# Kernel optimization log

Hardware: AMD Instinct MI355X
Metric: run time of the kernel (lower is better)

Reference implementation:

```python
import jax, jax.numpy as jnp
import numpy as np

N_USERS = 50000
N_ITEMS = 50000
E = 400000
S = 128   # in_feats_s (memory / GRU hidden)
T = 64    # in_feats_t (time encoding dim)
ED = 64   # edge feature dim
M = 2 * S + T + ED  # in_feats_m = 384

_BASIS_FREQ = jnp.asarray(1.0 / 10 ** np.linspace(0, 9, T), dtype=jnp.float32)


def time_encode(ts):
    # cos(ts * freq + phase), phase == 0
    return jnp.cos(ts[:, None] * _BASIS_FREQ[None, :])


def mean_message(src_mem, dst_mem, ts, e, src, dst, n_dst):
    # mail per edge: [E, 2S + T + ED]
    mail = jnp.concatenate(
        [src_mem[src], dst_mem[dst], time_encode(ts), e], axis=1)
    s = jax.ops.segment_sum(mail, dst, num_segments=n_dst)
    cnt = jax.ops.segment_sum(jnp.ones_like(ts), dst, num_segments=n_dst)
    return s / jnp.maximum(cnt, 1.0)[:, None]


def gru_step(x, h, w_ih, w_hh, b_ih, b_hh):
    # single-step PyTorch GRU; gate order r, z, n
    gi = x @ w_ih.T + b_ih
    gh = h @ w_hh.T + b_hh
    ir, iz, i_n = jnp.split(gi, 3, axis=1)
    hr, hz, h_n = jnp.split(gh, 3, axis=1)
    r = jax.nn.sigmoid(ir + hr)
    z = jax.nn.sigmoid(iz + hz)
    n = jnp.tanh(i_n + r * h_n)
    return (1.0 - z) * n + z * h


def setup_inputs() -> dict:
    key = jax.random.key(0)
    ks = jax.random.split(key, 16)
    sc = 1.0 / np.sqrt(S)
    return {
        "si":   jax.random.normal(ks[0], (N_USERS, S), jnp.float32),
        "sj":   jax.random.normal(ks[1], (N_ITEMS, S), jnp.float32),
        "si_r": jax.random.normal(ks[2], (N_ITEMS, S), jnp.float32),
        "sj_r": jax.random.normal(ks[3], (N_USERS, S), jnp.float32),
        "t":    jax.random.uniform(ks[4], (E,), jnp.float32),
        "t_r":  jax.random.uniform(ks[5], (E,), jnp.float32),
        "e":    jax.random.normal(ks[6], (E, ED), jnp.float32),
        "e_r":  jax.random.normal(ks[7], (E, ED), jnp.float32),
        "w_ih": jax.random.normal(ks[8], (3 * S, M), jnp.float32) * sc,
        "w_hh": jax.random.normal(ks[9], (3 * S, S), jnp.float32) * sc,
        "b_ih": jax.random.normal(ks[10], (3 * S,), jnp.float32) * sc,
        "b_hh": jax.random.normal(ks[11], (3 * S,), jnp.float32) * sc,
        "src_g":  jax.random.randint(ks[12], (E,), 0, N_USERS, jnp.int32),
        "dst_g":  jax.random.randint(ks[13], (E,), 0, N_ITEMS, jnp.int32),
        "src_gr": jax.random.randint(ks[14], (E,), 0, N_ITEMS, jnp.int32),
        "dst_gr": jax.random.randint(ks[15], (E,), 0, N_USERS, jnp.int32),
    }


def reference(si, sj, si_r, sj_r, t, t_r, e, e_r,
              w_ih, w_hh, b_ih, b_hh,
              src_g, dst_g, src_gr, dst_gr):
    # g: user -> item; g_r: item -> user
    mj = mean_message(si, sj, t, e, src_g, dst_g, N_ITEMS)       # messages to items
    mi = mean_message(si_r, sj_r, t_r, e_r, src_gr, dst_gr, N_USERS)  # messages to users
    si_out = gru_step(mi, sj_r, w_ih, w_hh, b_ih, b_hh)  # user memory update
    sj_out = gru_step(mj, sj, w_ih, w_hh, b_ih, b_hh)    # item memory update
    return (si_out, sj_out)
```

## Files before the change

kernel.cpp:

```cpp
#include <hip/hip_runtime.h>
#include <math.h>

#define NUSERS 50000
#define NITEMS 50000
#define NTOT   100000
#define NNODE  50000
#define NCHUNK 196
#define MTILES 6250
#define KDIM   512
#define NWAVES 8192

typedef __attribute__((ext_vector_type(4))) float f32x4;
typedef __attribute__((ext_vector_type(8))) short short8;
typedef unsigned int u32;

#define AS1 __attribute__((address_space(1)))
#define AS3 __attribute__((address_space(3)))

static __device__ __forceinline__ unsigned short f2bf(float f) {
  unsigned int u = __float_as_uint(f);
  u += 0x7fffu + ((u >> 16) & 1u);
  return (unsigned short)(u >> 16);
}

static __device__ __forceinline__ u32 pack2(float x, float y) {
  return (u32)f2bf(x) | ((u32)f2bf(y) << 16);
}

static __device__ __forceinline__ void gload_lds16(const void* g, void* l) {
  __builtin_amdgcn_global_load_lds((const AS1 u32*)g, (AS3 u32*)l, 16, 0, 0);
}

__global__ void pack_w_kernel(const float* __restrict__ w_ih,
                              const float* __restrict__ w_hh,
                              const float* __restrict__ b_ih,
                              const float* __restrict__ b_hh,
                              unsigned short* __restrict__ Wb,
                              float* __restrict__ bb) {
  int idx = blockIdx.x * 256 + threadIdx.x;
  int j = idx & 7, l = (idx >> 3) & 63, ktt = idx >> 9;
  int kt = ktt & 15, tt = ktt >> 4;
  int g = tt * 16 + (l & 15);
  int k = kt * 32 + (l >> 4) * 8 + j;
  float v;
  if (g < 256)      v = (k < 384) ? w_ih[g * 384 + k] : w_hh[g * 128 + (k - 384)];
  else if (g < 384) v = (k < 384) ? w_ih[g * 384 + k] : 0.0f;
  else              v = (k < 384) ? 0.0f : w_hh[(g - 128) * 128 + (k - 384)];
  Wb[idx] = f2bf(v);
  if (idx < 512) {
    float b = (idx < 256) ? (b_ih[idx] + b_hh[idx])
            : (idx < 384) ? b_ih[idx]
                          : b_hh[idx - 128];
    bb[idx] = b;
  }
}

__global__ void cast_mem_kernel(const float* __restrict__ si,
                                const float* __restrict__ si_r,
                                unsigned short* __restrict__ si_b,
                                unsigned short* __restrict__ sir_b) {
  int i = blockIdx.x * 256 + threadIdx.x;
  const float* src; unsigned short* dst; int off;
  if (i < 800000) { src = si;   dst = si_b;  off = i; }
  else            { src = si_r; dst = sir_b; off = i - 800000; }
  const f32x4* p = (const f32x4*)(src + (size_t)off * 8);
  f32x4 a = p[0], b = p[1];
  short8 o;
  o[0] = f2bf(a[0]); o[1] = f2bf(a[1]); o[2] = f2bf(a[2]); o[3] = f2bf(a[3]);
  o[4] = f2bf(b[0]); o[5] = f2bf(b[1]); o[6] = f2bf(b[2]); o[7] = f2bf(b[3]);
  *(short8*)(dst + (size_t)off * 8) = o;
}

__global__ void hist_kernel(const int* __restrict__ dst_g,
                            const int* __restrict__ dst_gr,
                            int* __restrict__ deg_j, int* __restrict__ deg_i, int E) {
  int i = blockIdx.x * 256 + threadIdx.x;
  if (i < E) atomicAdd(&deg_j[dst_g[i]], 1);
  else if (i < 2 * E) atomicAdd(&deg_i[dst_gr[i - E]], 1);
}

__global__ void chunksum_kernel(const int* __restrict__ deg_j,
                                const int* __restrict__ deg_i,
                                int* __restrict__ csum) {
  int c = blockIdx.x;
  const int* deg = (c < NCHUNK) ? deg_j : deg_i;
  int cc = (c < NCHUNK) ? c : c - NCHUNK;
  int t = threadIdx.x;
  int idx = cc * 256 + t;
  int v = (idx < NNODE) ? deg[idx] : 0;
  for (int off = 32; off; off >>= 1) v += __shfl_down(v, off, 64);
  __shared__ int wsum[4];
  if ((t & 63) == 0) wsum[t >> 6] = v;
  __syncthreads();
  if (t == 0) csum[c] = wsum[0] + wsum[1] + wsum[2] + wsum[3];
}

__global__ void chunkscan_kernel(const int* __restrict__ csum, int* __restrict__ coff) {
  int d = blockIdx.x;
  const int* cs = csum + d * NCHUNK;
  int* co = coff + d * NCHUNK;
  int t = threadIdx.x, lane = t & 63, w = t >> 6;
  int v = (t < NCHUNK) ? cs[t] : 0;
  int x = v;
  for (int off = 1; off < 64; off <<= 1) {
    int y = __shfl_up(x, off, 64);
    if (lane >= off) x += y;
  }
  __shared__ int wt[4];
  if (lane == 63) wt[w] = x;
  __syncthreads();
  int add = 0;
  for (int k = 0; k < 4; ++k) if (k < w) add += wt[k];
  if (t < NCHUNK) co[t] = add + x - v;
}

__global__ void localscan_kernel(const int* __restrict__ deg_j,
                                 const int* __restrict__ deg_i,
                                 const int* __restrict__ coff,
                                 int* __restrict__ rs_j, int* __restrict__ cur_j,
                                 int* __restrict__ rs_i, int* __restrict__ cur_i) {
  int c = blockIdx.x;
  bool dj = c < NCHUNK;
  const int* deg = dj ? deg_j : deg_i;
  int cc = dj ? c : c - NCHUNK;
  int* rs = dj ? rs_j : rs_i;
  int* cur = dj ? cur_j : cur_i;
  int base = coff[c];
  int t = threadIdx.x, lane = t & 63, w = t >> 6;
  int idx = cc * 256 + t;
  int v = (idx < NNODE) ? deg[idx] : 0;
  int x = v;
  for (int off = 1; off < 64; off <<= 1) {
    int y = __shfl_up(x, off, 64);
    if (lane >= off) x += y;
  }
  __shared__ int wt[4];
  if (lane == 63) wt[w] = x;
  __syncthreads();
  int add = 0;
  for (int k = 0; k < 4; ++k) if (k < w) add += wt[k];
  int ex = base + add + x - v;
  if (idx < NNODE) { rs[idx] = ex; cur[idx] = ex; }
}

__global__ void fill_kernel(const int* __restrict__ src_g, const int* __restrict__ dst_g,
                            const float* __restrict__ t,
                            const int* __restrict__ src_gr, const int* __restrict__ dst_gr,
                            const float* __restrict__ t_r,
                            int* __restrict__ cur_j, int* __restrict__ cur_i,
                            int4* __restrict__ recP_j, int4* __restrict__ recP_i,
                            int E) {
  int i = blockIdx.x * 256 + threadIdx.x;
  if (i < E) {
    int pos = atomicAdd(&cur_j[dst_g[i]], 1);
    recP_j[pos] = make_int4(src_g[i], i, __float_as_int(t[i]), 0);
  } else if (i < 2 * E) {
    int k = i - E;
    int pos = atomicAdd(&cur_i[dst_gr[k]], 1);
    recP_i[pos] = make_int4(src_gr[k], k, __float_as_int(t_r[k]), 0);
  }
}

__global__ __launch_bounds__(256) void gather_kernel(
    const unsigned short* __restrict__ si_b, const unsigned short* __restrict__ sir_b,
    const float* __restrict__ sj, const float* __restrict__ sj_r,
    const float* __restrict__ e, const float* __restrict__ e_r,
    const int* __restrict__ rs_j, const int* __restrict__ rs_i,
    const int* __restrict__ deg_j, const int* __restrict__ deg_i,
    const int4* __restrict__ recP_j, const int4* __restrict__ recP_i,
    unsigned short* __restrict__ Xb) {
  __shared__ __align__(16) unsigned short rowbuf[4][512];
  int wid = threadIdx.x >> 6, lane = threadIdx.x & 63;
  int gwave = blockIdx.x * 4 + wid;
  float freq = __expf((float)lane * -0.3289407276f);
  unsigned short* rb = rowbuf[wid];
  u32* rb32 = (u32*)rb;

  for (int node = gwave; node < NTOT; node += NWAVES) {
    bool user = node < NUSERS;
    int idx = user ? node : node - NUSERS;
    const unsigned short* smem = user ? sir_b : si_b;
    const float* h  = user ? sj_r : sj;
    const float* ef = user ? e_r : e;
    int start = __builtin_amdgcn_readfirstlane((user ? rs_i : rs_j)[idx]);
    int deg   = __builtin_amdgcn_readfirstlane((user ? deg_i : deg_j)[idx]);
    const int4* rec = user ? recP_i : recP_j;

    float2 hvf = *(const float2*)(h + (size_t)idx * 128 + 2 * lane);

    float asx = 0.f, asy = 0.f;
    float at  = 0.f;
    float ae  = 0.f;

    for (int base = 0; base < deg; base += 64) {
      int nn = deg - base; if (nn > 64) nn = 64;
      int cl = (lane < nn) ? base + lane : base + nn - 1;
      int4 r = rec[start + cl];
      int full = nn & ~7;
      for (int j0 = 0; j0 < full; j0 += 8) {
        int s0 = __builtin_amdgcn_readlane(r.x, j0 + 0), e0 = __builtin_amdgcn_readlane(r.y, j0 + 0);
        int s1 = __builtin_amdgcn_readlane(r.x, j0 + 1), e1 = __builtin_amdgcn_readlane(r.y, j0 + 1);
        int s2 = __builtin_amdgcn_readlane(r.x, j0 + 2), e2 = __builtin_amdgcn_readlane(r.y, j0 + 2);
        int s3 = __builtin_amdgcn_readlane(r.x, j0 + 3), e3 = __builtin_amdgcn_readlane(r.y, j0 + 3);
        int s4 = __builtin_amdgcn_readlane(r.x, j0 + 4), e4 = __builtin_amdgcn_readlane(r.y, j0 + 4);
        int s5 = __builtin_amdgcn_readlane(r.x, j0 + 5), e5 = __builtin_amdgcn_readlane(r.y, j0 + 5);
        int s6 = __builtin_amdgcn_readlane(r.x, j0 + 6), e6 = __builtin_amdgcn_readlane(r.y, j0 + 6);
        int s7 = __builtin_amdgcn_readlane(r.x, j0 + 7), e7 = __builtin_amdgcn_readlane(r.y, j0 + 7);

        u32 v0 = *(const u32*)(smem + ((size_t)s0 << 7) + 2 * lane);
        u32 v1 = *(const u32*)(smem + ((size_t)s1 << 7) + 2 * lane);
        u32 v2 = *(const u32*)(smem + ((size_t)s2 << 7) + 2 * lane);
        u32 v3 = *(const u32*)(smem + ((size_t)s3 << 7) + 2 * lane);
        u32 v4 = *(const u32*)(smem + ((size_t)s4 << 7) + 2 * lane);
        u32 v5 = *(const u32*)(smem + ((size_t)s5 << 7) + 2 * lane);
        u32 v6 = *(const u32*)(smem + ((size_t)s6 << 7) + 2 * lane);
        u32 v7 = *(const u32*)(smem + ((size_t)s7 << 7) + 2 * lane);
        float f0 = ef[((size_t)e0 << 6) + lane];
        float f1 = ef[((size_t)e1 << 6) + lane];
        float f2 = ef[((size_t)e2 << 6) + lane];
        float f3 = ef[((size_t)e3 << 6) + lane];
        float f4 = ef[((size_t)e4 << 6) + lane];
        float f5 = ef[((size_t)e5 << 6) + lane];
        float f6 = ef[((size_t)e6 << 6) + lane];
        float f7 = ef[((size_t)e7 << 6) + lane];

        float c0 = __cosf(__int_as_float(__builtin_amdgcn_readlane(r.z, j0 + 0)) * freq);
        float c1 = __cosf(__int_as_float(__builtin_amdgcn_readlane(r.z, j0 + 1)) * freq);
        float c2 = __cosf(__int_as_float(__builtin_amdgcn_readlane(r.z, j0 + 2)) * freq);
        float c3 = __cosf(__int_as_float(__builtin_amdgcn_readlane(r.z, j0 + 3)) * freq);
        float c4 = __cosf(__int_as_float(__builtin_amdgcn_readlane(r.z, j0 + 4)) * freq);
        float c5 = __cosf(__int_as_float(__builtin_amdgcn_readlane(r.z, j0 + 5)) * freq);
        float c6 = __cosf(__int_as_float(__builtin_amdgcn_readlane(r.z, j0 + 6)) * freq);
        float c7 = __cosf(__int_as_float(__builtin_amdgcn_readlane(r.z, j0 + 7)) * freq);

        float l0 = __uint_as_float(v0 << 16), g0 = __uint_as_float(v0 & 0xffff0000u);
        float l1 = __uint_as_float(v1 << 16), g1 = __uint_as_float(v1 & 0xffff0000u);
        float l2 = __uint_as_float(v2 << 16), g2 = __uint_as_float(v2 & 0xffff0000u);
        float l3 = __uint_as_float(v3 << 16), g3 = __uint_as_float(v3 & 0xffff0000u);
        float l4 = __uint_as_float(v4 << 16), g4 = __uint_as_float(v4 & 0xffff0000u);
        float l5 = __uint_as_float(v5 << 16), g5 = __uint_as_float(v5 & 0xffff0000u);
        float l6 = __uint_as_float(v6 << 16), g6 = __uint_as_float(v6 & 0xffff0000u);
        float l7 = __uint_as_float(v7 << 16), g7 = __uint_as_float(v7 & 0xffff0000u);

        asx += ((l0 + l1) + (l2 + l3)) + ((l4 + l5) + (l6 + l7));
        asy += ((g0 + g1) + (g2 + g3)) + ((g4 + g5) + (g6 + g7));
        at  += ((c0 + c1) + (c2 + c3)) + ((c4 + c5) + (c6 + c7));
        ae  += ((f0 + f1) + (f2 + f3)) + ((f4 + f5) + (f6 + f7));
      }
      if (full < nn) {
        int j0 = full;
        int j1 = (j0 + 1 < nn) ? j0 + 1 : nn - 1;
        int j2 = (j0 + 2 < nn) ? j0 + 2 : nn - 1;
        int j3 = (j0 + 3 < nn) ? j0 + 3 : nn - 1;
        int j4 = (j0 + 4 < nn) ? j0 + 4 : nn - 1;
        int j5 = (j0 + 5 < nn) ? j0 + 5 : nn - 1;
        int j6 = (j0 + 6 < nn) ? j0 + 6 : nn - 1;
        float w1 = (j0 + 1 < nn) ? 1.0f : 0.0f;
        float w2 = (j0 + 2 < nn) ? 1.0f : 0.0f;
        float w3 = (j0 + 3 < nn) ? 1.0f : 0.0f;
        float w4 = (j0 + 4 < nn) ? 1.0f : 0.0f;
        float w5 = (j0 + 5 < nn) ? 1.0f : 0.0f;
        float w6 = (j0 + 6 < nn) ? 1.0f : 0.0f;

        int s0 = __builtin_amdgcn_readlane(r.x, j0), e0 = __builtin_amdgcn_readlane(r.y, j0);
        int s1 = __builtin_amdgcn_readlane(r.x, j1), e1 = __builtin_amdgcn_readlane(r.y, j1);
        int s2 = __builtin_amdgcn_readlane(r.x, j2), e2 = __builtin_amdgcn_readlane(r.y, j2);
        int s3 = __builtin_amdgcn_readlane(r.x, j3), e3 = __builtin_amdgcn_readlane(r.y, j3);
        int s4 = __builtin_amdgcn_readlane(r.x, j4), e4 = __builtin_amdgcn_readlane(r.y, j4);
        int s5 = __builtin_amdgcn_readlane(r.x, j5), e5 = __builtin_amdgcn_readlane(r.y, j5);
        int s6 = __builtin_amdgcn_readlane(r.x, j6), e6 = __builtin_amdgcn_readlane(r.y, j6);

        u32 v0 = *(const u32*)(smem + ((size_t)s0 << 7) + 2 * lane);
        u32 v1 = *(const u32*)(smem + ((size_t)s1 << 7) + 2 * lane);
        u32 v2 = *(const u32*)(smem + ((size_t)s2 << 7) + 2 * lane);
        u32 v3 = *(const u32*)(smem + ((size_t)s3 << 7) + 2 * lane);
        u32 v4 = *(const u32*)(smem + ((size_t)s4 << 7) + 2 * lane);
        u32 v5 = *(const u32*)(smem + ((size_t)s5 << 7) + 2 * lane);
        u32 v6 = *(const u32*)(smem + ((size_t)s6 << 7) + 2 * lane);
        float f0 = ef[((size_t)e0 << 6) + lane];
        float f1 = ef[((size_t)e1 << 6) + lane];
        float f2 = ef[((size_t)e2 << 6) + lane];
        float f3 = ef[((size_t)e3 << 6) + lane];
        float f4 = ef[((size_t)e4 << 6) + lane];
        float f5 = ef[((size_t)e5 << 6) + lane];
        float f6 = ef[((size_t)e6 << 6) + lane];

        float c0 = __cosf(__int_as_float(__builtin_amdgcn_readlane(r.z, j0)) * freq);
        float c1 = __cosf(__int_as_float(__builtin_amdgcn_readlane(r.z, j1)) * freq);
        float c2 = __cosf(__int_as_float(__builtin_amdgcn_readlane(r.z, j2)) * freq);
        float c3 = __cosf(__int_as_float(__builtin_amdgcn_readlane(r.z, j3)) * freq);
        float c4 = __cosf(__int_as_float(__builtin_amdgcn_readlane(r.z, j4)) * freq);
        float c5 = __cosf(__int_as_float(__builtin_amdgcn_readlane(r.z, j5)) * freq);
        float c6 = __cosf(__int_as_float(__builtin_amdgcn_readlane(r.z, j6)) * freq);

        float l0 = __uint_as_float(v0 << 16), g0 = __uint_as_float(v0 & 0xffff0000u);
        float l1 = __uint_as_float(v1 << 16), g1 = __uint_as_float(v1 & 0xffff0000u);
        float l2 = __uint_as_float(v2 << 16), g2 = __uint_as_float(v2 & 0xffff0000u);
        float l3 = __uint_as_float(v3 << 16), g3 = __uint_as_float(v3 & 0xffff0000u);
        float l4 = __uint_as_float(v4 << 16), g4 = __uint_as_float(v4 & 0xffff0000u);
        float l5 = __uint_as_float(v5 << 16), g5 = __uint_as_float(v5 & 0xffff0000u);
        float l6 = __uint_as_float(v6 << 16), g6 = __uint_as_float(v6 & 0xffff0000u);

        asx += l0 + w1 * l1 + w2 * l2 + w3 * l3 + w4 * l4 + w5 * l5 + w6 * l6;
        asy += g0 + w1 * g1 + w2 * g2 + w3 * g3 + w4 * g4 + w5 * g5 + w6 * g6;
        at  += c0 + w1 * c1 + w2 * c2 + w3 * c3 + w4 * c4 + w5 * c5 + w6 * c6;
        ae  += f0 + w1 * f1 + w2 * f2 + w3 * f3 + w4 * f4 + w5 * f5 + w6 * f6;
      }
    }

    float invc = (deg > 0) ? 1.0f / (float)deg : 0.0f;
    float hz   = (deg > 0) ? 1.0f : 0.0f;

    rb32[lane]       = pack2(asx * invc, asy * invc);
    rb32[64 + lane]  = pack2(hvf.x * hz, hvf.y * hz);
    rb[256 + lane]   = f2bf(at * invc);
    rb[320 + lane]   = f2bf(ae * invc);
    rb32[192 + lane] = pack2(hvf.x, hvf.y);

    short8 vv = *(const short8*)(rb + lane * 8);
    *(short8*)(Xb + (size_t)node * 512 + lane * 8) = vv;
  }
}

__global__ __launch_bounds__(512, 3) void gemm_gru_kernel(
    const unsigned short* __restrict__ Xb,
    const unsigned short* __restrict__ Wb,
    const float* __restrict__ bb,
    const float* __restrict__ sj_r,
    const float* __restrict__ sj,
    float* __restrict__ out) {
  int wid = threadIdx.x >> 6, lane = threadIdx.x & 63;
  int mbase = blockIdx.x * 4;
  int col16 = lane & 15, quad = lane >> 4;

  f32x4 acc[4][4];
#pragma unroll
  for (int mi = 0; mi < 4; ++mi)
#pragma unroll
    for (int g = 0; g < 4; ++g) acc[mi][g] = (f32x4)0.0f;

  int mt[4];
  const unsigned short* Ap[4];
#pragma unroll
  for (int mi = 0; mi < 4; ++mi) {
    mt[mi] = mbase + mi;
    int mc = (mt[mi] < MTILES) ? mt[mi] : MTILES - 1;
    Ap[mi] = Xb + (size_t)(mc * 16 + col16) * 512 + quad * 8;
  }
  const unsigned short* Bp[4];
#pragma unroll
  for (int g = 0; g < 4; ++g)
    Bp[g] = Wb + ((size_t)(g * 8 + wid) * 16 * 64 + lane) * 8;

#pragma unroll
  for (int kt = 0; kt < 16; ++kt) {
    short8 a[4], b[4];
#pragma unroll
    for (int mi = 0; mi < 4; ++mi) a[mi] = *(const short8*)(Ap[mi] + kt * 32);
#pragma unroll
    for (int g = 0; g < 4; ++g)    b[g]  = *(const short8*)(Bp[g] + (size_t)kt * 512);
#pragma unroll
    for (int mi = 0; mi < 4; ++mi)
#pragma unroll
      for (int g = 0; g < 4; ++g)
        acc[mi][g] = __builtin_amdgcn_mfma_f32_16x16x32_bf16(a[mi], b[g], acc[mi][g], 0, 0, 0);
  }

  int cc = wid * 16 + col16;
  float bbr = bb[cc], bbz = bb[128 + cc], bbn = bb[256 + cc], bbh = bb[384 + cc];
#pragma unroll
  for (int mi = 0; mi < 4; ++mi) {
    if (mt[mi] >= MTILES) continue;
#pragma unroll
    for (int r = 0; r < 4; ++r) {
      int row = mt[mi] * 16 + quad * 4 + r;
      float rp  = acc[mi][0][r] + bbr;
      float zp  = acc[mi][1][r] + bbz;
      float inp = acc[mi][2][r] + bbn;
      float hnp = acc[mi][3][r] + bbh;
      float rg = 1.0f / (1.0f + __expf(-rp));
      float zg = 1.0f / (1.0f + __expf(-zp));
      float ng = tanhf(inp + rg * hnp);
      float hv = (row < NUSERS) ? sj_r[(size_t)row * 128 + cc]
                                : sj[(size_t)(row - NUSERS) * 128 + cc];
      out[(size_t)row * 128 + cc] = (1.0f - zg) * ng + zg * hv;
    }
  }
}

extern "C" void kernel_launch(void* const* d_in, const int* in_sizes, int n_in,
                              void* d_out, int out_size, void* d_ws, size_t ws_size,
                              hipStream_t stream) {
  const float* si   = (const float*)d_in[0];
  const float* sj   = (const float*)d_in[1];
  const float* si_r = (const float*)d_in[2];
  const float* sj_r = (const float*)d_in[3];
  const float* t    = (const float*)d_in[4];
  const float* t_r  = (const float*)d_in[5];
  const float* e    = (const float*)d_in[6];
  const float* e_r  = (const float*)d_in[7];
  const float* w_ih = (const float*)d_in[8];
  const float* w_hh = (const float*)d_in[9];
  const float* b_ih = (const float*)d_in[10];
  const float* b_hh = (const float*)d_in[11];
  const int* src_g  = (const int*)d_in[12];
  const int* dst_g  = (const int*)d_in[13];
  const int* src_gr = (const int*)d_in[14];
  const int* dst_gr = (const int*)d_in[15];
  int E = in_sizes[4];

  unsigned short* Xb = (unsigned short*)d_ws;
  unsigned short* Wb = Xb + (size_t)NTOT * 512;
  float* bb   = (float*)(Wb + 262144);
  int* deg_j  = (int*)(bb + 512);
  int* deg_i  = deg_j + NNODE;
  int* rs_j   = deg_i + NNODE;
  int* rs_i   = rs_j + NNODE;
  int* cur_j  = rs_i + NNODE;
  int* cur_i  = cur_j + NNODE;
  int* csum   = cur_i + NNODE;
  int* coff   = csum + 2 * NCHUNK;
  int4* recP_j = (int4*)(coff + 2 * NCHUNK);
  int4* recP_i = recP_j + E;
  unsigned short* si_b  = (unsigned short*)(recP_i + E);
  unsigned short* sir_b = si_b + 6400000;

  hipMemsetAsync(deg_j, 0, 2 * NNODE * sizeof(int), stream);

  pack_w_kernel<<<(512 * 512) / 256, 256, 0, stream>>>(w_ih, w_hh, b_ih, b_hh, Wb, bb);
  cast_mem_kernel<<<6250, 256, 0, stream>>>(si, si_r, si_b, sir_b);

  int blks2E = (2 * E + 255) / 256;
  hist_kernel<<<blks2E, 256, 0, stream>>>(dst_g, dst_gr, deg_j, deg_i, E);
  chunksum_kernel<<<2 * NCHUNK, 256, 0, stream>>>(deg_j, deg_i, csum);
  chunkscan_kernel<<<2, 256, 0, stream>>>(csum, coff);
  localscan_kernel<<<2 * NCHUNK, 256, 0, stream>>>(deg_j, deg_i, coff, rs_j, cur_j, rs_i, cur_i);
  fill_kernel<<<blks2E, 256, 0, stream>>>(src_g, dst_g, t, src_gr, dst_gr, t_r,
                                          cur_j, cur_i, recP_j, recP_i, E);

  gather_kernel<<<NWAVES / 4, 256, 0, stream>>>(si_b, sir_b, sj, sj_r, e, e_r,
                                                rs_j, rs_i, deg_j, deg_i,
                                                recP_j, recP_i, Xb);

  float* out = (float*)d_out;
  gemm_gru_kernel<<<(MTILES + 3) / 4, 512, 0, stream>>>(Xb, Wb, bb, sj_r, sj, out);
}
```

Before: 653.1 us.

## Stage GEMM tiles through double-buffered LDS with 8 M-tiles per block

```diff
diff --git a/kernel.cpp b/kernel.cpp
--- a/kernel.cpp
+++ b/kernel.cpp
@@ -322,68 +322,83 @@
   }
 }
 
-__global__ __launch_bounds__(512, 3) void gemm_gru_kernel(
+__global__ __launch_bounds__(512) void gemm_gru_kernel(
     const unsigned short* __restrict__ Xb,
     const unsigned short* __restrict__ Wb,
     const float* __restrict__ bb,
     const float* __restrict__ sj_r,
     const float* __restrict__ sj,
     float* __restrict__ out) {
+  __shared__ __align__(16) unsigned short sA[2][4096];
+  __shared__ __align__(16) unsigned short sB[2][16384];
   int wid = threadIdx.x >> 6, lane = threadIdx.x & 63;
-  int mbase = blockIdx.x * 4;
+  int mg = wid >> 2, cg = wid & 3;
+  int mbase = blockIdx.x * 8;
   int col16 = lane & 15, quad = lane >> 4;
 
-  f32x4 acc[4][4];
+  int mts = mbase + wid; if (mts >= MTILES) mts = MTILES - 1;
+  const unsigned short* gA = Xb + (size_t)(mts * 16 + col16) * 512 + quad * 8;
+  const unsigned short* gB = Wb + ((size_t)(wid * 4) * 16 * 64 + lane) * 8;
+
+#define STAGE9(buf, kt)                                                       \
+  {                                                                           \
+    gload_lds16(gA + (kt) * 32, sA[buf] + wid * 512);                         \
+    _Pragma("unroll")                                                         \
+    for (int i = 0; i < 4; ++i)                                               \
+      gload_lds16(gB + ((size_t)(i * 16 + (kt))) * 512, sB[buf] + (wid * 4 + i) * 512); \
+  }
+
+  f32x4 acc[4][8];
 #pragma unroll
   for (int mi = 0; mi < 4; ++mi)
 #pragma unroll
-    for (int g = 0; g < 4; ++g) acc[mi][g] = (f32x4)0.0f;
-
-  int mt[4];
-  const unsigned short* Ap[4];
-#pragma unroll
-  for (int mi = 0; mi < 4; ++mi) {
-    mt[mi] = mbase + mi;
-    int mc = (mt[mi] < MTILES) ? mt[mi] : MTILES - 1;
-    Ap[mi] = Xb + (size_t)(mc * 16 + col16) * 512 + quad * 8;
-  }
-  const unsigned short* Bp[4];
-#pragma unroll
-  for (int g = 0; g < 4; ++g)
-    Bp[g] = Wb + ((size_t)(g * 8 + wid) * 16 * 64 + lane) * 8;
-
-#pragma unroll
+    for (int t8 = 0; t8 < 8; ++t8) acc[mi][t8] = (f32x4)0.0f;
+
+  STAGE9(0, 0)
+  __syncthreads();
+
   for (int kt = 0; kt < 16; ++kt) {
-    short8 a[4], b[4];
-#pragma unroll
-    for (int mi = 0; mi < 4; ++mi) a[mi] = *(const short8*)(Ap[mi] + kt * 32);
-#pragma unroll
-    for (int g = 0; g < 4; ++g)    b[g]  = *(const short8*)(Bp[g] + (size_t)kt * 512);
+    int cur = kt & 1;
+    if (kt < 15) STAGE9(cur ^ 1, kt + 1)
+    short8 a[4], b[8];
 #pragma unroll
     for (int mi = 0; mi < 4; ++mi)
-#pragma unroll
-      for (int g = 0; g < 4; ++g)
-        acc[mi][g] = __builtin_amdgcn_mfma_f32_16x16x32_bf16(a[mi], b[g], acc[mi][g], 0, 0, 0);
-  }
-
-  int cc = wid * 16 + col16;
-  float bbr = bb[cc], bbz = bb[128 + cc], bbn = bb[256 + cc], bbh = bb[384 + cc];
-#pragma unroll
-  for (int mi = 0; mi < 4; ++mi) {
-    if (mt[mi] >= MTILES) continue;
-#pragma unroll
-    for (int r = 0; r < 4; ++r) {
-      int row = mt[mi] * 16 + quad * 4 + r;
-      float rp  = acc[mi][0][r] + bbr;
-      float zp  = acc[mi][1][r] + bbz;
-      float inp = acc[mi][2][r] + bbn;
-      float hnp = acc[mi][3][r] + bbh;
-      float rg = 1.0f / (1.0f + __expf(-rp));
-      float zg = 1.0f / (1.0f + __expf(-zp));
-      float ng = tanhf(inp + rg * hnp);
-      float hv = (row < NUSERS) ? sj_r[(size_t)row * 128 + cc]
-                                : sj[(size_t)(row - NUSERS) * 128 + cc];
-      out[(size_t)row * 128 + cc] = (1.0f - zg) * ng + zg * hv;
+      a[mi] = *(const short8*)(sA[cur] + (mg * 4 + mi) * 512 + lane * 8);
+#pragma unroll
+    for (int g = 0; g < 4; ++g)
+#pragma unroll
+      for (int nt = 0; nt < 2; ++nt)
+        b[g * 2 + nt] = *(const short8*)(sB[cur] + (g * 8 + cg * 2 + nt) * 512 + lane * 8);
+#pragma unroll
+    for (int mi = 0; mi < 4; ++mi)
+#pragma unroll
+      for (int t8 = 0; t8 < 8; ++t8)
+        acc[mi][t8] = __builtin_amdgcn_mfma_f32_16x16x32_bf16(a[mi], b[t8], acc[mi][t8], 0, 0, 0);
+    __syncthreads();
+  }
+
+#pragma unroll
+  for (int nt = 0; nt < 2; ++nt) {
+    int cc = (cg * 2 + nt) * 16 + col16;
+    float bbr = bb[cc], bbz = bb[128 + cc], bbn = bb[256 + cc], bbh = bb[384 + cc];
+#pragma unroll
+    for (int mi = 0; mi < 4; ++mi) {
+      int mt = mbase + mg * 4 + mi;
+      if (mt >= MTILES) continue;
+#pragma unroll
+      for (int r = 0; r < 4; ++r) {
+        int row = mt * 16 + quad * 4 + r;
+        float rp  = acc[mi][0 + nt][r] + bbr;
+        float zp  = acc[mi][2 + nt][r] + bbz;
+        float inp = acc[mi][4 + nt][r] + bbn;
+        float hnp = acc[mi][6 + nt][r] + bbh;
+        float rg = 1.0f / (1.0f + __expf(-rp));
+        float zg = 1.0f / (1.0f + __expf(-zp));
+        float ng = tanhf(inp + rg * hnp);
+        float hv = (row < NUSERS) ? sj_r[(size_t)row * 128 + cc]
+                                  : sj[(size_t)(row - NUSERS) * 128 + cc];
+        out[(size_t)row * 128 + cc] = (1.0f - zg) * ng + zg * hv;
+      }
     }
   }
 }
@@ -443,5 +458,5 @@
                                                 recP_j, recP_i, Xb);
 
   float* out = (float*)d_out;
-  gemm_gru_kernel<<<(MTILES + 3) / 4, 512, 0, stream>>>(Xb, Wb, bb, sj_r, sj, out);
-}
+  gemm_gru_kernel<<<(MTILES + 7) / 8, 512, 0, stream>>>(Xb, Wb, bb, sj_r, sj, out);
+}
```

Measured after the change: 622.3 us. 1.05x faster.
